# Kernel tuning notes

Measured on AMD Instinct MI355X. Metric: run time of the kernel, lower is better.

The kernel has to match this reference:

```python
import jax, jax.numpy as jnp
import numpy as np

EPS = 0.001  # numerical_stabilizer


def setup_inputs() -> dict:
    key = jax.random.key(0)
    ks = jax.random.split(key, 8)
    B, L, D, H, M = 4, 4096, 1024, 16, 64
    scale = 0.02
    return {
        "query": jax.random.normal(ks[0], (B, L, D), jnp.float32),
        "key": jax.random.normal(ks[1], (B, L, D), jnp.float32),
        "value": jax.random.normal(ks[2], (B, L, D), jnp.float32),
        "Wq": jax.random.normal(ks[3], (D, H, M), jnp.float32) * scale,
        "bq": jnp.zeros((H, M), jnp.float32),
        "Wk": jax.random.normal(ks[4], (D, H, M), jnp.float32) * scale,
        "bk": jnp.zeros((H, M), jnp.float32),
        "Wv": jax.random.normal(ks[5], (D, H, M), jnp.float32) * scale,
        "bv": jnp.zeros((H, M), jnp.float32),
        "Wo": jax.random.normal(ks[6], (H, M, D), jnp.float32) * scale,
        "bo": jnp.zeros((D,), jnp.float32),
        "step": 0,
    }


def reference(query, key, value, Wq, bq, Wk, bk, Wv, bv, Wo, bo, step):
    # QKV projections: [B,L,D] x [D,H,M] -> [B,L,H,M]
    q = jnp.einsum('bld,dhm->blhm', query, Wq) + bq
    k = jnp.einsum('bld,dhm->blhm', key, Wk) + bk
    v = jnp.einsum('bld,dhm->blhm', value, Wv) + bv
    # ReLU feature map with stabilizer
    q = jax.nn.relu(q) + EPS
    k = jax.nn.relu(k) + EPS
    # Linear (kernelized) attention: KV outer-product state [B,H,M,M]
    kvs = jnp.einsum('blhm,blhd->bhmd', k, v)
    a_v = jnp.einsum('blhm,bhmd->blhd', q, kvs)
    # Normalizer: sum of keys over sequence
    ks_sum = jnp.sum(k, axis=1)                       # [B,H,M]
    norm = jnp.einsum('blhm,bhm->blh', q, ks_sum)     # [B,L,H]
    a_v = a_v / norm[..., None]
    # Output projection over (head, head_dim) -> hidden
    out = jnp.einsum('blhm,hmd->bld', a_v, Wo) + bo
    return out
```

## Files before the change

### kernel.cpp

```cpp
#include <hip/hip_runtime.h>
#include <stdint.h>


typedef __bf16 bf16;
typedef __bf16 bf16x4 __attribute__((ext_vector_type(4)));
typedef __bf16 bf16x8 __attribute__((ext_vector_type(8)));
typedef float f32x4 __attribute__((ext_vector_type(4)));

#define MFMA_(a, b, c) __builtin_amdgcn_mfma_f32_16x16x32_bf16((a), (b), (c), 0, 0, 0)

static constexpr int BB   = 4;
static constexpr int LSEQ = 4096;
static constexpr int DIM  = 1024;
static constexpr int HH   = 16;
static constexpr float EPSF = 0.001f;

__device__ __forceinline__ void gload16(bf16* lds, const bf16* g) {
  __builtin_amdgcn_global_load_lds(
      (const __attribute__((address_space(1))) void*)g,
      (__attribute__((address_space(3))) void*)lds, 16, 0, 0);
}

__global__ void k_cvt(const float* __restrict__ q, const float* __restrict__ k,
                      const float* __restrict__ v, bf16* __restrict__ xb) {
  const int nchunk = 3 << 21;
  const int nthr = gridDim.x * blockDim.x;
  int c = blockIdx.x * blockDim.x + threadIdx.x;
  for (; c + nthr < nchunk; c += 2 * nthr) {
    const int c2 = c + nthr;
    const int t1 = c >> 21, t2 = c2 >> 21;
    const size_t o1 = (size_t)(c  & 0x1FFFFF) * 8;
    const size_t o2 = (size_t)(c2 & 0x1FFFFF) * 8;
    const float* s1 = (t1 == 0) ? q : (t1 == 1) ? k : v;
    const float* s2 = (t2 == 0) ? q : (t2 == 1) ? k : v;
    const f32x4 a0 = __builtin_nontemporal_load(reinterpret_cast<const f32x4*>(s1 + o1));
    const f32x4 a1 = __builtin_nontemporal_load(reinterpret_cast<const f32x4*>(s1 + o1) + 1);
    const f32x4 b0 = __builtin_nontemporal_load(reinterpret_cast<const f32x4*>(s2 + o2));
    const f32x4 b1 = __builtin_nontemporal_load(reinterpret_cast<const f32x4*>(s2 + o2) + 1);
    bf16x8 oa, ob;
#pragma unroll
    for (int j = 0; j < 4; ++j) { oa[j] = (bf16)a0[j]; oa[4 + j] = (bf16)a1[j]; }
#pragma unroll
    for (int j = 0; j < 4; ++j) { ob[j] = (bf16)b0[j]; ob[4 + j] = (bf16)b1[j]; }
    *reinterpret_cast<bf16x8*>(xb + (size_t)t1 * 16777216u + o1) = oa;
    *reinterpret_cast<bf16x8*>(xb + (size_t)t2 * 16777216u + o2) = ob;
  }
  if (c < nchunk) {
    const int t = c >> 21;
    const size_t off = (size_t)(c & 0x1FFFFF) * 8;
    const float* src = (t == 0) ? q : (t == 1) ? k : v;
    const f32x4 a = __builtin_nontemporal_load(reinterpret_cast<const f32x4*>(src + off));
    const f32x4 b = __builtin_nontemporal_load(reinterpret_cast<const f32x4*>(src + off) + 1);
    bf16x8 o;
#pragma unroll
    for (int j = 0; j < 4; ++j) { o[j] = (bf16)a[j]; o[4 + j] = (bf16)b[j]; }
    *reinterpret_cast<bf16x8*>(xb + (size_t)t * 16777216u + off) = o;
  }
}

__global__ void k_prep_w4(const float* __restrict__ W0, const float* __restrict__ W1,
                          const float* __restrict__ W2, const float* __restrict__ W3,
                          bf16* __restrict__ T0, bf16* __restrict__ T1,
                          bf16* __restrict__ T2, bf16* __restrict__ T3) {
  const float* W; bf16* T;
  switch (blockIdx.z) {
    case 0:  W = W0; T = T0; break;
    case 1:  W = W1; T = T1; break;
    case 2:  W = W2; T = T2; break;
    default: W = W3; T = T3; break;
  }
  __shared__ float t[32][33];
  const int tx = threadIdx.x & 31, ty = threadIdx.x >> 5;
  const int r0 = blockIdx.x * 32, c0 = blockIdx.y * 32;
#pragma unroll
  for (int j = 0; j < 32; j += 8)
    t[ty + j][tx] = W[(size_t)(r0 + ty + j) * DIM + c0 + tx];
  __syncthreads();
#pragma unroll
  for (int j = 0; j < 32; j += 8)
    T[(size_t)(c0 + ty + j) * DIM + r0 + tx] = (bf16)t[tx][ty + j];
}

__global__ void k_init_vt(bf16* __restrict__ vt) {
  const int c = blockIdx.x * 256 + threadIdx.x;
  const int l8 = c & 511;
  const int r  = (c >> 9) & 15;
  const int bh = c >> 13;
  const bf16 val = (r == 0) ? (bf16)1.0f : (bf16)0.0f;
  bf16x8 o;
#pragma unroll
  for (int j = 0; j < 8; ++j) o[j] = val;
  *reinterpret_cast<bf16x8*>(vt + ((size_t)bh * 80 + 64 + r) * LSEQ + l8 * 8) = o;
}

__device__ __forceinline__ void stage_half(bf16* As0, bf16* Bs0,
                                           const bf16* Ab, const bf16* Bb,
                                           int h, int w, int srow, int scol) {
  const int t = h >> 2, reg = h & 3, buf = t & 1;
  bf16* lds = ((reg < 2) ? As0 : Bs0) + buf * 16384 + (reg & 1) * 8192;
  const bf16* g = (reg < 2) ? Ab : Bb;
  const int rbase = (reg & 1) * 128;
#pragma unroll
  for (int rr = 0; rr < 2; ++rr) {
    const int row = rbase + (rr * 8 + w) * 8 + srow;
    gload16(lds + (rr * 8 + w) * 512, g + (size_t)row * DIM + t * 64 + scol);
  }
}

#define LDA(d, g, f)                                                                              \
  a[d][0] = *reinterpret_cast<const bf16x8*>(&As0[(g) * 16384 + (wm * 128 + (f) * 16 + lr) * 64 + col0]); \
  a[d][1] = *reinterpret_cast<const bf16x8*>(&As0[(g) * 16384 + (wm * 128 + (f) * 16 + lr) * 64 + col1]);
#define LDB(d, g, c)                                                                              \
  b[d][0] = *reinterpret_cast<const bf16x8*>(&Bs0[(g) * 16384 + (wn * 64 + (c) * 16 + lr) * 64 + col0]); \
  b[d][1] = *reinterpret_cast<const bf16x8*>(&Bs0[(g) * 16384 + (wn * 64 + (c) * 16 + lr) * 64 + col1]);
#define MM(fi, ci, fo, co)                                                                        \
  acc[fo][co] = MFMA_(a[fi][0], b[ci][0], acc[fo][co]);                                           \
  acc[fo][co] = MFMA_(a[fi][1], b[ci][1], acc[fo][co]);

#define PHASE(g, q, pidx)                                                                         \
  {                                                                                               \
    if ((q) == 0) { LDA(0, g, 0) LDA(1, g, 1) LDA(2, g, 2) LDA(3, g, 3)                           \
                    LDB(0, g, 0) LDB(1, g, 1) }                                                   \
    else if ((q) == 1) { LDB(0, g, 2) LDB(1, g, 3) }                                              \
    else if ((q) == 2) { LDA(0, g, 4) LDA(1, g, 5) LDA(2, g, 6) LDA(3, g, 7) }                    \
    else { LDB(0, g, 0) LDB(1, g, 1) }                                                            \
    const int hh = 8 * i + 5 + (pidx);                                                            \
    if (hh < 64) stage_half(As0, Bs0, Ab, Bb, hh, w, srow, scol);                                 \
    if ((pidx) == 3 || (pidx) == 7) {                                                             \
      if (i < 7) { asm volatile("s_waitcnt vmcnt(2)" ::: "memory"); }                             \
      else       { asm volatile("s_waitcnt vmcnt(0)" ::: "memory"); }                             \
    }                                                                                             \
    __builtin_amdgcn_sched_barrier(0);                                                            \
    __builtin_amdgcn_s_barrier();                                                                 \
    __builtin_amdgcn_sched_barrier(0);                                                            \
    __builtin_amdgcn_s_setprio(1);                                                                \
    if ((q) == 0) { MM(0, 0, 0, 0) MM(1, 0, 1, 0) MM(2, 0, 2, 0) MM(3, 0, 3, 0)                   \
                    MM(0, 1, 0, 1) MM(1, 1, 1, 1) MM(2, 1, 2, 1) MM(3, 1, 3, 1) }                 \
    else if ((q) == 1) { MM(0, 0, 0, 2) MM(1, 0, 1, 2) MM(2, 0, 2, 2) MM(3, 0, 3, 2)              \
                         MM(0, 1, 0, 3) MM(1, 1, 1, 3) MM(2, 1, 2, 3) MM(3, 1, 3, 3) }            \
    else if ((q) == 2) { MM(0, 0, 4, 2) MM(1, 0, 5, 2) MM(2, 0, 6, 2) MM(3, 0, 7, 2)              \
                         MM(0, 1, 4, 3) MM(1, 1, 5, 3) MM(2, 1, 6, 3) MM(3, 1, 7, 3) }            \
    else { MM(0, 0, 4, 0) MM(1, 0, 5, 0) MM(2, 0, 6, 0) MM(3, 0, 7, 0)                            \
           MM(0, 1, 4, 1) MM(1, 1, 5, 1) MM(2, 1, 6, 1) MM(3, 1, 7, 1) }                          \
    __builtin_amdgcn_s_setprio(0);                                                                \
    __builtin_amdgcn_sched_barrier(0);                                                            \
    __builtin_amdgcn_s_barrier();                                                                 \
    __builtin_amdgcn_sched_barrier(0);                                                            \
  }

template <int MODE>
__global__ __launch_bounds__(512, 2) void k_gemm256(const bf16* __restrict__ X,
                                                    const bf16* __restrict__ WT,
                                                    const float* __restrict__ bias,
                                                    void* __restrict__ outp) {
  __shared__ __align__(16) bf16 SH[65536];
  bf16* As0 = SH;
  bf16* Bs0 = SH + 32768;
  const int tid = threadIdx.x;
  const int lane = tid & 63, w = tid >> 6;
  const int wm = w >> 2, wn = w & 3;
  const int lr = lane & 15, lk = (lane >> 4) & 3;
  const int n0 = blockIdx.x * 256, c0 = blockIdx.y * 256;
  const int swz = (lr & 7) * 8;
  const int col0 = (lk * 8) ^ swz;
  const int col1 = (lk * 8 + 32) ^ swz;
  const int srow = lane >> 3;
  const int scol = (((lane & 7) ^ ((lane >> 3) & 7)) * 8);
  const bf16* Ab = X + (size_t)n0 * DIM;
  const bf16* Bb = WT + (size_t)c0 * DIM;

  f32x4 acc[8][4] = {};
  bf16x8 a[4][2], b[2][2];

#pragma unroll
  for (int h = 0; h < 5; ++h) stage_half(As0, Bs0, Ab, Bb, h, w, srow, scol);
  asm volatile("s_waitcnt vmcnt(2)" ::: "memory");
  __builtin_amdgcn_sched_barrier(0);
  __builtin_amdgcn_s_barrier();
  __builtin_amdgcn_sched_barrier(0);

  for (int i = 0; i < 8; ++i) {
    PHASE(0, 0, 0) PHASE(0, 1, 1) PHASE(0, 2, 2) PHASE(0, 3, 3)
    PHASE(1, 0, 4) PHASE(1, 1, 5) PHASE(1, 2, 6) PHASE(1, 3, 7)
  }

  float bvv[4];
#pragma unroll
  for (int cb = 0; cb < 4; ++cb) bvv[cb] = bias[c0 + wn * 64 + cb * 16 + lr];
  const int bidx = n0 >> 12;
  const int l0 = n0 & (LSEQ - 1);

  if (MODE == 3) {
    float* out = (float*)outp;
#pragma unroll
    for (int f = 0; f < 8; ++f)
#pragma unroll
      for (int cb = 0; cb < 4; ++cb) {
        const int c = c0 + wn * 64 + cb * 16 + lr;
#pragma unroll
        for (int r = 0; r < 4; ++r) {
          const int row = n0 + wm * 128 + f * 16 + lk * 4 + r;
          out[(size_t)row * DIM + c] = acc[f][cb][r] + bvv[cb];
        }
      }
  } else if (MODE == 0) {
    __syncthreads();
#pragma unroll
    for (int f = 0; f < 8; ++f)
#pragma unroll
      for (int cb = 0; cb < 4; ++cb) {
        const int cl = wn * 64 + cb * 16 + lr;
#pragma unroll
        for (int r = 0; r < 4; ++r) {
          float x = acc[f][cb][r] + bvv[cb];
          x = fmaxf(x, 0.f) + EPSF;
          const int ll = wm * 128 + f * 16 + lk * 4 + r;
          SH[ll * 256 + ((((cl >> 3) ^ (ll & 7)) << 3) | (cl & 7))] = (bf16)x;
        }
      }
    __syncthreads();
    bf16* outb = (bf16*)outp;
#pragma unroll
    for (int it = 0; it < 16; ++it) {
      const int chunk = it * 512 + tid;
      const int row = chunk >> 5, blk = chunk & 31;
      const bf16x8 v = *reinterpret_cast<const bf16x8*>(&SH[row * 256 + ((blk ^ (row & 7)) << 3)]);
      *reinterpret_cast<bf16x8*>(outb + (size_t)(n0 + row) * DIM + c0 + blk * 8) = v;
    }
  } else {
    __syncthreads();
#pragma unroll
    for (int f = 0; f < 8; ++f)
#pragma unroll
      for (int cb = 0; cb < 4; ++cb) {
        const int cl = wn * 64 + cb * 16 + lr;
        const int ll = wm * 128 + f * 16 + lk * 4;
        bf16x4 o;
#pragma unroll
        for (int r = 0; r < 4; ++r) {
          float x = acc[f][cb][r] + bvv[cb];
          if (MODE == 1) x = fmaxf(x, 0.f) + EPSF;
          o[r] = (bf16)x;
        }
        *reinterpret_cast<bf16x4*>(
            &SH[cl * 256 + ((((ll >> 3) ^ (cl & 7)) << 3) | (ll & 7))]) = o;
      }
    __syncthreads();
    bf16* outb = (bf16*)outp;
#pragma unroll
    for (int it = 0; it < 16; ++it) {
      const int chunk = it * 512 + tid;
      const int row = chunk >> 5, blk = chunk & 31;
      const bf16x8 v = *reinterpret_cast<const bf16x8*>(&SH[row * 256 + ((blk ^ (row & 7)) << 3)]);
      const int cg = c0 + row;
      size_t rowbase;
      if (MODE == 1) rowbase = (size_t)bidx * 1024 + cg;
      else           rowbase = ((size_t)(bidx * HH + (cg >> 6)) * 80 + (cg & 63));
      *reinterpret_cast<bf16x8*>(outb + rowbase * LSEQ + l0 + blk * 8) = v;
    }
  }
}
#undef PHASE
#undef MM
#undef LDB
#undef LDA

__global__ __launch_bounds__(256, 2) void k_kvs(const bf16* __restrict__ kt,
                                                const bf16* __restrict__ vt,
                                                float* __restrict__ kvs) {
  const int tid = threadIdx.x, lane = tid & 63, wid = tid >> 6;
  const int lr = lane & 15, lk = lane >> 4;
  const int bh = blockIdx.y;
  const int lbase = blockIdx.x * 256;
  __shared__ bf16 As[64][64];
  __shared__ bf16 Bs[80][64];
  f32x4 acc[5] = {};
  const bf16* ktb = kt + (size_t)bh * 64 * LSEQ;
  const bf16* vtb = vt + (size_t)bh * 80 * LSEQ;

  for (int ks = 0; ks < 4; ++ks) {
    const int l0 = lbase + ks * 64;
    __syncthreads();
#pragma unroll
    for (int i = 0; i < 2; ++i) {
      const int e = i * 2048 + tid * 8;
      const int row = e >> 6, col = e & 63;
      *reinterpret_cast<bf16x8*>(&As[row][col]) =
          *reinterpret_cast<const bf16x8*>(ktb + (size_t)row * LSEQ + l0 + col);
    }
#pragma unroll
    for (int i = 0; i < 2; ++i) {
      const int e = i * 2048 + tid * 8;
      const int row = e >> 6, col = e & 63;
      *reinterpret_cast<bf16x8*>(&Bs[row][col]) =
          *reinterpret_cast<const bf16x8*>(vtb + (size_t)row * LSEQ + l0 + col);
    }
    if (tid < 128) {
      const int e = 4096 + tid * 8;
      const int row = e >> 6, col = e & 63;
      *reinterpret_cast<bf16x8*>(&Bs[row][col]) =
          *reinterpret_cast<const bf16x8*>(vtb + (size_t)row * LSEQ + l0 + col);
    }
    __syncthreads();
#pragma unroll
    for (int kk = 0; kk < 2; ++kk) {
      const bf16x8 af = *reinterpret_cast<const bf16x8*>(&As[wid * 16 + lr][kk * 32 + lk * 8]);
#pragma unroll
      for (int cb = 0; cb < 5; ++cb) {
        const bf16x8 bfr = *reinterpret_cast<const bf16x8*>(&Bs[cb * 16 + lr][kk * 32 + lk * 8]);
        acc[cb] = MFMA_(af, bfr, acc[cb]);
      }
    }
  }
  float* kb = kvs + (size_t)bh * 64 * 80;
#pragma unroll
  for (int cb = 0; cb < 5; ++cb) {
    const int dcol = cb * 16 + lr;
#pragma unroll
    for (int r = 0; r < 4; ++r) {
      const int m = wid * 16 + lk * 4 + r;
      atomicAdd(kb + m * 80 + dcol, acc[cb][r]);
    }
  }
}

__global__ void k_kvs_t(const float* __restrict__ kvs, bf16* __restrict__ bav) {
  const int bh = blockIdx.x;
  const float* src = kvs + (size_t)bh * 5120;
  bf16* dst = bav + (size_t)bh * 5120;
  for (int i = threadIdx.x; i < 5120; i += 256) {
    const int dp = i >> 6, mm = i & 63;
    dst[i] = (bf16)src[mm * 80 + dp];
  }
}

__global__ __launch_bounds__(256, 2) void k_av(const bf16* __restrict__ q,
                                               const bf16* __restrict__ bav,
                                               bf16* __restrict__ avn) {
  const int tid = threadIdx.x, lane = tid & 63, wid = tid >> 6;
  const int lr = lane & 15, lk = lane >> 4;
  const int bh = blockIdx.y, b = bh >> 4, h = bh & 15;
  const int l0 = blockIdx.x * 128;
  __shared__ bf16 As[128][64];
  __shared__ bf16 Bs[80][64];
  __shared__ float nrm[128];

  const bf16* qb = q + ((size_t)b * LSEQ + l0) * DIM + h * 64;
#pragma unroll
  for (int i = 0; i < 4; ++i) {
    const int e = i * 2048 + tid * 8;
    const int row = e >> 6, col = e & 63;
    *reinterpret_cast<bf16x8*>(&As[row][col]) =
        *reinterpret_cast<const bf16x8*>(qb + (size_t)row * DIM + col);
  }
  const bf16* bb = bav + (size_t)bh * 5120;
#pragma unroll
  for (int i = 0; i < 2; ++i) {
    const int e = i * 2048 + tid * 8;
    const int row = e >> 6, col = e & 63;
    *reinterpret_cast<bf16x8*>(&Bs[row][col]) =
        *reinterpret_cast<const bf16x8*>(bb + row * 64 + col);
  }
  if (tid < 128) {
    const int e = 4096 + tid * 8;
    const int row = e >> 6, col = e & 63;
    *reinterpret_cast<bf16x8*>(&Bs[row][col]) =
        *reinterpret_cast<const bf16x8*>(bb + row * 64 + col);
  }
  __syncthreads();

  f32x4 acc[2][5] = {};
#pragma unroll
  for (int kk = 0; kk < 2; ++kk) {
    bf16x8 af[2];
    af[0] = *reinterpret_cast<const bf16x8*>(&As[wid * 32 + lr][kk * 32 + lk * 8]);
    af[1] = *reinterpret_cast<const bf16x8*>(&As[wid * 32 + 16 + lr][kk * 32 + lk * 8]);
#pragma unroll
    for (int cb = 0; cb < 5; ++cb) {
      const bf16x8 bfr = *reinterpret_cast<const bf16x8*>(&Bs[cb * 16 + lr][kk * 32 + lk * 8]);
      acc[0][cb] = MFMA_(af[0], bfr, acc[0][cb]);
      acc[1][cb] = MFMA_(af[1], bfr, acc[1][cb]);
    }
  }
  if (lr == 0) {
#pragma unroll
    for (int rb = 0; rb < 2; ++rb)
#pragma unroll
      for (int r = 0; r < 4; ++r)
        nrm[wid * 32 + rb * 16 + lk * 4 + r] = acc[rb][4][r];
  }
  __syncthreads();
  bf16* ob = avn + ((size_t)b * LSEQ + l0) * DIM + h * 64;
#pragma unroll
  for (int rb = 0; rb < 2; ++rb) {
#pragma unroll
    for (int cb = 0; cb < 4; ++cb) {
#pragma unroll
      for (int r = 0; r < 4; ++r) {
        const int row = wid * 32 + rb * 16 + lk * 4 + r;
        const float x = acc[rb][cb][r] / nrm[row];
        ob[(size_t)row * DIM + cb * 16 + lr] = (bf16)x;
      }
    }
  }
}

extern "C" void kernel_launch(void* const* d_in, const int* in_sizes, int n_in,
                              void* d_out, int out_size, void* d_ws, size_t ws_size,
                              hipStream_t stream) {
  const float* query = (const float*)d_in[0];
  const float* key   = (const float*)d_in[1];
  const float* value = (const float*)d_in[2];
  const float* Wq    = (const float*)d_in[3];
  const float* bq    = (const float*)d_in[4];
  const float* Wk    = (const float*)d_in[5];
  const float* bk    = (const float*)d_in[6];
  const float* Wv    = (const float*)d_in[7];
  const float* bvp   = (const float*)d_in[8];
  const float* Wo    = (const float*)d_in[9];
  const float* bo    = (const float*)d_in[10];
  float* out = (float*)d_out;
  char* ws = (char*)d_ws;

  const size_t off_wqt = 0;
  const size_t off_wkt = off_wqt + (2u << 20);
  const size_t off_wvt = off_wkt + (2u << 20);
  const size_t off_wot = off_wvt + (2u << 20);
  const size_t off_xb  = off_wot + (2u << 20);
  const size_t off_vt  = off_xb  + 100663296ull;
  const size_t off_kvs = off_vt  + 41943040ull;
  const size_t off_bav = off_kvs + 1310720ull;
  const size_t total   = off_bav + 655360ull;
  if (ws_size < total) return;

  bf16*  WQT = (bf16*)(ws + off_wqt);
  bf16*  WKT = (bf16*)(ws + off_wkt);
  bf16*  WVT = (bf16*)(ws + off_wvt);
  bf16*  WOT = (bf16*)(ws + off_wot);
  bf16*  XB  = (bf16*)(ws + off_xb);
  bf16*  XBq = XB;
  bf16*  XBk = XB + 16777216u;
  bf16*  XBv = XB + 33554432u;
  bf16*  VT  = (bf16*)(ws + off_vt);
  float* KVS = (float*)(ws + off_kvs);
  bf16*  BAV = (bf16*)(ws + off_bav);
  bf16*  KT  = XBv;
  bf16*  Qb  = XBk;
  bf16*  AV  = XBq;

  k_cvt<<<2048, 256, 0, stream>>>(query, key, value, XB);
  k_prep_w4<<<dim3(32, 32, 4), 256, 0, stream>>>(Wq, Wk, Wv, Wo, WQT, WKT, WVT, WOT);
  k_init_vt<<<2048, 256, 0, stream>>>(VT);
  (void)hipMemsetAsync(KVS, 0, 1310720ull, stream);

  k_gemm256<2><<<dim3(64, 4), 512, 0, stream>>>(XBv, WVT, bvp, VT);
  k_gemm256<1><<<dim3(64, 4), 512, 0, stream>>>(XBk, WKT, bk, KT);
  k_gemm256<0><<<dim3(64, 4), 512, 0, stream>>>(XBq, WQT, bq, Qb);

  k_kvs<<<dim3(16, 64), 256, 0, stream>>>(KT, VT, KVS);
  k_kvs_t<<<64, 256, 0, stream>>>(KVS, BAV);

  k_av<<<dim3(32, 64), 256, 0, stream>>>(Qb, BAV, AV);

  k_gemm256<3><<<dim3(64, 4), 512, 0, stream>>>(AV, WOT, bo, out);
}
```

Measured before the change: 256.8 us.

## Deepen GEMM prefetch, hold full A/B fragments in registers, simplify convert loop

The 256x256 GEMM mainloop now loads all 8 A fragments and 4 B fragments into registers in the first two phases, so the later phases issue MFMAs with no LDS reads. The prefetch distance grows from 5 to 7 half-tiles, with the vmcnt waits changed to match, and stage_half now stages B before A. The aim is to cut LDS read traffic and hide more global-load latency. This raises register pressure under launch_bounds(512,2), which could cause spills or lower occupancy. The input conversion kernel also drops its manual two-chunk unrolling in favour of a plain grid-stride loop.

```diff
diff --git a/kernel.cpp b/kernel.cpp
--- a/kernel.cpp
+++ b/kernel.cpp
@@ -24,36 +24,17 @@
 __global__ void k_cvt(const float* __restrict__ q, const float* __restrict__ k,
                       const float* __restrict__ v, bf16* __restrict__ xb) {
   const int nchunk = 3 << 21;
-  const int nthr = gridDim.x * blockDim.x;
-  int c = blockIdx.x * blockDim.x + threadIdx.x;
-  for (; c + nthr < nchunk; c += 2 * nthr) {
-    const int c2 = c + nthr;
-    const int t1 = c >> 21, t2 = c2 >> 21;
-    const size_t o1 = (size_t)(c  & 0x1FFFFF) * 8;
-    const size_t o2 = (size_t)(c2 & 0x1FFFFF) * 8;
-    const float* s1 = (t1 == 0) ? q : (t1 == 1) ? k : v;
-    const float* s2 = (t2 == 0) ? q : (t2 == 1) ? k : v;
-    const f32x4 a0 = __builtin_nontemporal_load(reinterpret_cast<const f32x4*>(s1 + o1));
-    const f32x4 a1 = __builtin_nontemporal_load(reinterpret_cast<const f32x4*>(s1 + o1) + 1);
-    const f32x4 b0 = __builtin_nontemporal_load(reinterpret_cast<const f32x4*>(s2 + o2));
-    const f32x4 b1 = __builtin_nontemporal_load(reinterpret_cast<const f32x4*>(s2 + o2) + 1);
-    bf16x8 oa, ob;
-#pragma unroll
-    for (int j = 0; j < 4; ++j) { oa[j] = (bf16)a0[j]; oa[4 + j] = (bf16)a1[j]; }
-#pragma unroll
-    for (int j = 0; j < 4; ++j) { ob[j] = (bf16)b0[j]; ob[4 + j] = (bf16)b1[j]; }
-    *reinterpret_cast<bf16x8*>(xb + (size_t)t1 * 16777216u + o1) = oa;
-    *reinterpret_cast<bf16x8*>(xb + (size_t)t2 * 16777216u + o2) = ob;
-  }
-  if (c < nchunk) {
+  const int stride = gridDim.x * blockDim.x;
+  for (int c = blockIdx.x * blockDim.x + threadIdx.x; c < nchunk; c += stride) {
     const int t = c >> 21;
-    const size_t off = (size_t)(c & 0x1FFFFF) * 8;
+    const size_t off = (size_t)(c & ((1 << 21) - 1)) * 8;
     const float* src = (t == 0) ? q : (t == 1) ? k : v;
-    const f32x4 a = __builtin_nontemporal_load(reinterpret_cast<const f32x4*>(src + off));
-    const f32x4 b = __builtin_nontemporal_load(reinterpret_cast<const f32x4*>(src + off) + 1);
+    const f32x4* sp = reinterpret_cast<const f32x4*>(src + off);
+    const f32x4 a = __builtin_nontemporal_load(sp);
+    const f32x4 b = __builtin_nontemporal_load(sp + 1);
     bf16x8 o;
-#pragma unroll
-    for (int j = 0; j < 4; ++j) { o[j] = (bf16)a[j]; o[4 + j] = (bf16)b[j]; }
+    o[0] = (bf16)a[0]; o[1] = (bf16)a[1]; o[2] = (bf16)a[2]; o[3] = (bf16)a[3];
+    o[4] = (bf16)b[0]; o[5] = (bf16)b[1]; o[6] = (bf16)b[2]; o[7] = (bf16)b[3];
     *reinterpret_cast<bf16x8*>(xb + (size_t)t * 16777216u + off) = o;
   }
 }
@@ -97,8 +78,8 @@
                                            const bf16* Ab, const bf16* Bb,
                                            int h, int w, int srow, int scol) {
   const int t = h >> 2, reg = h & 3, buf = t & 1;
-  bf16* lds = ((reg < 2) ? As0 : Bs0) + buf * 16384 + (reg & 1) * 8192;
-  const bf16* g = (reg < 2) ? Ab : Bb;
+  bf16* lds = ((reg >= 2) ? As0 : Bs0) + buf * 16384 + (reg & 1) * 8192;
+  const bf16* g = (reg >= 2) ? Ab : Bb;
   const int rbase = (reg & 1) * 128;
 #pragma unroll
   for (int rr = 0; rr < 2; ++rr) {
@@ -120,14 +101,12 @@
 #define PHASE(g, q, pidx)                                                                         \
   {                                                                                               \
     if ((q) == 0) { LDA(0, g, 0) LDA(1, g, 1) LDA(2, g, 2) LDA(3, g, 3)                           \
-                    LDB(0, g, 0) LDB(1, g, 1) }                                                   \
-    else if ((q) == 1) { LDB(0, g, 2) LDB(1, g, 3) }                                              \
-    else if ((q) == 2) { LDA(0, g, 4) LDA(1, g, 5) LDA(2, g, 6) LDA(3, g, 7) }                    \
-    else { LDB(0, g, 0) LDB(1, g, 1) }                                                            \
-    const int hh = 8 * i + 5 + (pidx);                                                            \
+                    LDB(0, g, 0) LDB(1, g, 1) LDB(2, g, 2) LDB(3, g, 3) }                         \
+    else if ((q) == 1) { LDA(4, g, 4) LDA(5, g, 5) LDA(6, g, 6) LDA(7, g, 7) }                    \
+    const int hh = 8 * i + 7 + (pidx);                                                            \
     if (hh < 64) stage_half(As0, Bs0, Ab, Bb, hh, w, srow, scol);                                 \
     if ((pidx) == 3 || (pidx) == 7) {                                                             \
-      if (i < 7) { asm volatile("s_waitcnt vmcnt(2)" ::: "memory"); }                             \
+      if (i < 7) { asm volatile("s_waitcnt vmcnt(6)" ::: "memory"); }                             \
       else       { asm volatile("s_waitcnt vmcnt(0)" ::: "memory"); }                             \
     }                                                                                             \
     __builtin_amdgcn_sched_barrier(0);                                                            \
@@ -136,12 +115,12 @@
     __builtin_amdgcn_s_setprio(1);                                                                \
     if ((q) == 0) { MM(0, 0, 0, 0) MM(1, 0, 1, 0) MM(2, 0, 2, 0) MM(3, 0, 3, 0)                   \
                     MM(0, 1, 0, 1) MM(1, 1, 1, 1) MM(2, 1, 2, 1) MM(3, 1, 3, 1) }                 \
-    else if ((q) == 1) { MM(0, 0, 0, 2) MM(1, 0, 1, 2) MM(2, 0, 2, 2) MM(3, 0, 3, 2)              \
-                         MM(0, 1, 0, 3) MM(1, 1, 1, 3) MM(2, 1, 2, 3) MM(3, 1, 3, 3) }            \
-    else if ((q) == 2) { MM(0, 0, 4, 2) MM(1, 0, 5, 2) MM(2, 0, 6, 2) MM(3, 0, 7, 2)              \
-                         MM(0, 1, 4, 3) MM(1, 1, 5, 3) MM(2, 1, 6, 3) MM(3, 1, 7, 3) }            \
-    else { MM(0, 0, 4, 0) MM(1, 0, 5, 0) MM(2, 0, 6, 0) MM(3, 0, 7, 0)                            \
-           MM(0, 1, 4, 1) MM(1, 1, 5, 1) MM(2, 1, 6, 1) MM(3, 1, 7, 1) }                          \
+    else if ((q) == 1) { MM(0, 2, 0, 2) MM(1, 2, 1, 2) MM(2, 2, 2, 2) MM(3, 2, 3, 2)              \
+                         MM(0, 3, 0, 3) MM(1, 3, 1, 3) MM(2, 3, 2, 3) MM(3, 3, 3, 3) }            \
+    else if ((q) == 2) { MM(4, 2, 4, 2) MM(5, 2, 5, 2) MM(6, 2, 6, 2) MM(7, 2, 7, 2)              \
+                         MM(4, 3, 4, 3) MM(5, 3, 5, 3) MM(6, 3, 6, 3) MM(7, 3, 7, 3) }            \
+    else { MM(4, 0, 4, 0) MM(5, 0, 5, 0) MM(6, 0, 6, 0) MM(7, 0, 7, 0)                            \
+           MM(4, 1, 4, 1) MM(5, 1, 5, 1) MM(6, 1, 6, 1) MM(7, 1, 7, 1) }                          \
     __builtin_amdgcn_s_setprio(0);                                                                \
     __builtin_amdgcn_sched_barrier(0);                                                            \
     __builtin_amdgcn_s_barrier();                                                                 \
@@ -170,11 +149,11 @@
   const bf16* Bb = WT + (size_t)c0 * DIM;
 
   f32x4 acc[8][4] = {};
-  bf16x8 a[4][2], b[2][2];
-
-#pragma unroll
-  for (int h = 0; h < 5; ++h) stage_half(As0, Bs0, Ab, Bb, h, w, srow, scol);
-  asm volatile("s_waitcnt vmcnt(2)" ::: "memory");
+  bf16x8 a[8][2], b[4][2];
+
+#pragma unroll
+  for (int h = 0; h < 7; ++h) stage_half(As0, Bs0, Ab, Bb, h, w, srow, scol);
+  asm volatile("s_waitcnt vmcnt(6)" ::: "memory");
   __builtin_amdgcn_sched_barrier(0);
   __builtin_amdgcn_s_barrier();
   __builtin_amdgcn_sched_barrier(0);
```

Result: slower. 286.4 us (+11.5%).

## Fuse fp32-to-bf16 input conversion into the QKV projection GEMMs

Applied to the files above, without the earlier changes.

Removes the standalone conversion kernel that turned query, key and value into bf16 in a workspace buffer. A new projection GEMM instead loads the fp32 activations straight into registers, converts them, and writes the bf16 tile into swizzled LDS, while the weights still use async global-to-LDS loads. The aim is to drop the extra full write and re-read of the converted activations. In exchange, the fp32 inputs are fetched once per column block, twice the bytes per fetch. The new kernel also uses a simpler single-buffer loop with register prefetch instead of the tuned ping-pong MFMA pipeline.

```diff
diff --git a/kernel.cpp b/kernel.cpp
--- a/kernel.cpp
+++ b/kernel.cpp
@@ -19,43 +19,6 @@
   __builtin_amdgcn_global_load_lds(
       (const __attribute__((address_space(1))) void*)g,
       (__attribute__((address_space(3))) void*)lds, 16, 0, 0);
-}
-
-__global__ void k_cvt(const float* __restrict__ q, const float* __restrict__ k,
-                      const float* __restrict__ v, bf16* __restrict__ xb) {
-  const int nchunk = 3 << 21;
-  const int nthr = gridDim.x * blockDim.x;
-  int c = blockIdx.x * blockDim.x + threadIdx.x;
-  for (; c + nthr < nchunk; c += 2 * nthr) {
-    const int c2 = c + nthr;
-    const int t1 = c >> 21, t2 = c2 >> 21;
-    const size_t o1 = (size_t)(c  & 0x1FFFFF) * 8;
-    const size_t o2 = (size_t)(c2 & 0x1FFFFF) * 8;
-    const float* s1 = (t1 == 0) ? q : (t1 == 1) ? k : v;
-    const float* s2 = (t2 == 0) ? q : (t2 == 1) ? k : v;
-    const f32x4 a0 = __builtin_nontemporal_load(reinterpret_cast<const f32x4*>(s1 + o1));
-    const f32x4 a1 = __builtin_nontemporal_load(reinterpret_cast<const f32x4*>(s1 + o1) + 1);
-    const f32x4 b0 = __builtin_nontemporal_load(reinterpret_cast<const f32x4*>(s2 + o2));
-    const f32x4 b1 = __builtin_nontemporal_load(reinterpret_cast<const f32x4*>(s2 + o2) + 1);
-    bf16x8 oa, ob;
-#pragma unroll
-    for (int j = 0; j < 4; ++j) { oa[j] = (bf16)a0[j]; oa[4 + j] = (bf16)a1[j]; }
-#pragma unroll
-    for (int j = 0; j < 4; ++j) { ob[j] = (bf16)b0[j]; ob[4 + j] = (bf16)b1[j]; }
-    *reinterpret_cast<bf16x8*>(xb + (size_t)t1 * 16777216u + o1) = oa;
-    *reinterpret_cast<bf16x8*>(xb + (size_t)t2 * 16777216u + o2) = ob;
-  }
-  if (c < nchunk) {
-    const int t = c >> 21;
-    const size_t off = (size_t)(c & 0x1FFFFF) * 8;
-    const float* src = (t == 0) ? q : (t == 1) ? k : v;
-    const f32x4 a = __builtin_nontemporal_load(reinterpret_cast<const f32x4*>(src + off));
-    const f32x4 b = __builtin_nontemporal_load(reinterpret_cast<const f32x4*>(src + off) + 1);
-    bf16x8 o;
-#pragma unroll
-    for (int j = 0; j < 4; ++j) { o[j] = (bf16)a[j]; o[4 + j] = (bf16)b[j]; }
-    *reinterpret_cast<bf16x8*>(xb + (size_t)t * 16777216u + off) = o;
-  }
 }
 
 __global__ void k_prep_w4(const float* __restrict__ W0, const float* __restrict__ W1,
@@ -91,6 +54,146 @@
 #pragma unroll
   for (int j = 0; j < 8; ++j) o[j] = val;
   *reinterpret_cast<bf16x8*>(vt + ((size_t)bh * 80 + 64 + r) * LSEQ + l8 * 8) = o;
+}
+
+template <int MODE>
+__global__ __launch_bounds__(512, 2) void k_projf(const float* __restrict__ X,
+                                                  const bf16* __restrict__ WT,
+                                                  const float* __restrict__ bias,
+                                                  bf16* __restrict__ outp) {
+  __shared__ __align__(16) bf16 SH[65536];
+  bf16* As = SH;
+  bf16* Bs = SH + 16384;
+  const int tid = threadIdx.x;
+  const int lane = tid & 63, w = tid >> 6;
+  const int wm = w >> 2, wn = w & 3;
+  const int lr = lane & 15, lk = (lane >> 4) & 3;
+  const int n0 = blockIdx.x * 256, c0 = blockIdx.y * 256;
+  const int swz = (lr & 7) * 8;
+  const int col0 = (lk * 8) ^ swz;
+  const int col1 = (lk * 8 + 32) ^ swz;
+  const int srow = lane >> 3;
+  const int scol = (((lane & 7) ^ ((lane >> 3) & 7)) * 8);
+  const float* Xb = X + (size_t)n0 * DIM;
+  const bf16* Bb = WT + (size_t)c0 * DIM;
+
+  f32x4 acc[8][4] = {};
+  f32x4 af[8];
+  const int arow[1] = {0};  (void)arow;
+
+#pragma unroll
+  for (int j = 0; j < 8; ++j) {
+    const int idx = tid + j * 512, row = idx >> 4, c4 = idx & 15;
+    af[j] = __builtin_nontemporal_load(
+        reinterpret_cast<const f32x4*>(Xb + (size_t)row * DIM + c4 * 4));
+  }
+
+  for (int ks = 0; ks < 16; ++ks) {
+    const int k0 = ks * 64;
+    __syncthreads();
+#pragma unroll
+    for (int rr = 0; rr < 4; ++rr) {
+      const int row = (rr * 8 + w) * 8 + srow;
+      gload16(Bs + (rr * 8 + w) * 512, Bb + (size_t)row * DIM + k0 + scol);
+    }
+#pragma unroll
+    for (int j = 0; j < 8; ++j) {
+      const int idx = tid + j * 512, row = idx >> 4, c4 = idx & 15;
+      bf16x4 o;
+      o[0] = (bf16)af[j][0]; o[1] = (bf16)af[j][1];
+      o[2] = (bf16)af[j][2]; o[3] = (bf16)af[j][3];
+      *reinterpret_cast<bf16x4*>(
+          &As[row * 64 + ((((c4 >> 1) ^ (row & 7)) << 3) | ((c4 & 1) << 2))]) = o;
+    }
+    __syncthreads();
+    if (ks < 15) {
+#pragma unroll
+      for (int j = 0; j < 8; ++j) {
+        const int idx = tid + j * 512, row = idx >> 4, c4 = idx & 15;
+        af[j] = __builtin_nontemporal_load(
+            reinterpret_cast<const f32x4*>(Xb + (size_t)row * DIM + k0 + 64 + c4 * 4));
+      }
+    }
+    bf16x8 a[8][2], b[4][2];
+#pragma unroll
+    for (int f = 0; f < 8; ++f) {
+      a[f][0] = *reinterpret_cast<const bf16x8*>(&As[(wm * 128 + f * 16 + lr) * 64 + col0]);
+      a[f][1] = *reinterpret_cast<const bf16x8*>(&As[(wm * 128 + f * 16 + lr) * 64 + col1]);
+    }
+#pragma unroll
+    for (int cb = 0; cb < 4; ++cb) {
+      b[cb][0] = *reinterpret_cast<const bf16x8*>(&Bs[(wn * 64 + cb * 16 + lr) * 64 + col0]);
+      b[cb][1] = *reinterpret_cast<const bf16x8*>(&Bs[(wn * 64 + cb * 16 + lr) * 64 + col1]);
+    }
+#pragma unroll
+    for (int kk = 0; kk < 2; ++kk)
+#pragma unroll
+      for (int f = 0; f < 8; ++f)
+#pragma unroll
+        for (int cb = 0; cb < 4; ++cb)
+          acc[f][cb] = MFMA_(a[f][kk], b[cb][kk], acc[f][cb]);
+  }
+
+  float bvv[4];
+#pragma unroll
+  for (int cb = 0; cb < 4; ++cb) bvv[cb] = bias[c0 + wn * 64 + cb * 16 + lr];
+  const int bidx = n0 >> 12;
+  const int l0 = n0 & (LSEQ - 1);
+
+  if (MODE == 0) {
+    __syncthreads();
+#pragma unroll
+    for (int f = 0; f < 8; ++f)
+#pragma unroll
+      for (int cb = 0; cb < 4; ++cb) {
+        const int cl = wn * 64 + cb * 16 + lr;
+#pragma unroll
+        for (int r = 0; r < 4; ++r) {
+          float x = acc[f][cb][r] + bvv[cb];
+          x = fmaxf(x, 0.f) + EPSF;
+          const int ll = wm * 128 + f * 16 + lk * 4 + r;
+          SH[ll * 256 + ((((cl >> 3) ^ (ll & 7)) << 3) | (cl & 7))] = (bf16)x;
+        }
+      }
+    __syncthreads();
+#pragma unroll
+    for (int it = 0; it < 16; ++it) {
+      const int chunk = it * 512 + tid;
+      const int row = chunk >> 5, blk = chunk & 31;
+      const bf16x8 v = *reinterpret_cast<const bf16x8*>(&SH[row * 256 + ((blk ^ (row & 7)) << 3)]);
+      *reinterpret_cast<bf16x8*>(outp + (size_t)(n0 + row) * DIM + c0 + blk * 8) = v;
+    }
+  } else {
+    __syncthreads();
+#pragma unroll
+    for (int f = 0; f < 8; ++f)
+#pragma unroll
+      for (int cb = 0; cb < 4; ++cb) {
+        const int cl = wn * 64 + cb * 16 + lr;
+        const int ll = wm * 128 + f * 16 + lk * 4;
+        bf16x4 o;
+#pragma unroll
+        for (int r = 0; r < 4; ++r) {
+          float x = acc[f][cb][r] + bvv[cb];
+          if (MODE == 1) x = fmaxf(x, 0.f) + EPSF;
+          o[r] = (bf16)x;
+        }
+        *reinterpret_cast<bf16x4*>(
+            &SH[cl * 256 + ((((ll >> 3) ^ (cl & 7)) << 3) | (ll & 7))]) = o;
+      }
+    __syncthreads();
+#pragma unroll
+    for (int it = 0; it < 16; ++it) {
+      const int chunk = it * 512 + tid;
+      const int row = chunk >> 5, blk = chunk & 31;
+      const bf16x8 v = *reinterpret_cast<const bf16x8*>(&SH[row * 256 + ((blk ^ (row & 7)) << 3)]);
+      const int cg = c0 + row;
+      size_t rowbase;
+      if (MODE == 1) rowbase = (size_t)bidx * 1024 + cg;
+      else           rowbase = ((size_t)(bidx * HH + (cg >> 6)) * 80 + (cg & 63));
+      *reinterpret_cast<bf16x8*>(outp + rowbase * LSEQ + l0 + blk * 8) = v;
+    }
+  }
 }
 
 __device__ __forceinline__ void stage_half(bf16* As0, bf16* Bs0,
@@ -148,11 +251,10 @@
     __builtin_amdgcn_sched_barrier(0);                                                            \
   }
 
-template <int MODE>
 __global__ __launch_bounds__(512, 2) void k_gemm256(const bf16* __restrict__ X,
                                                     const bf16* __restrict__ WT,
                                                     const float* __restrict__ bias,
-                                                    void* __restrict__ outp) {
+                                                    float* __restrict__ outp) {
   __shared__ __align__(16) bf16 SH[65536];
   bf16* As0 = SH;
   bf16* Bs0 = SH + 32768;
@@ -187,78 +289,17 @@
   float bvv[4];
 #pragma unroll
   for (int cb = 0; cb < 4; ++cb) bvv[cb] = bias[c0 + wn * 64 + cb * 16 + lr];
-  const int bidx = n0 >> 12;
-  const int l0 = n0 & (LSEQ - 1);
-
-  if (MODE == 3) {
-    float* out = (float*)outp;
-#pragma unroll
-    for (int f = 0; f < 8; ++f)
-#pragma unroll
-      for (int cb = 0; cb < 4; ++cb) {
-        const int c = c0 + wn * 64 + cb * 16 + lr;
-#pragma unroll
-        for (int r = 0; r < 4; ++r) {
-          const int row = n0 + wm * 128 + f * 16 + lk * 4 + r;
-          out[(size_t)row * DIM + c] = acc[f][cb][r] + bvv[cb];
-        }
+#pragma unroll
+  for (int f = 0; f < 8; ++f)
+#pragma unroll
+    for (int cb = 0; cb < 4; ++cb) {
+      const int c = c0 + wn * 64 + cb * 16 + lr;
+#pragma unroll
+      for (int r = 0; r < 4; ++r) {
+        const int row = n0 + wm * 128 + f * 16 + lk * 4 + r;
+        outp[(size_t)row * DIM + c] = acc[f][cb][r] + bvv[cb];
       }
-  } else if (MODE == 0) {
-    __syncthreads();
-#pragma unroll
-    for (int f = 0; f < 8; ++f)
-#pragma unroll
-      for (int cb = 0; cb < 4; ++cb) {
-        const int cl = wn * 64 + cb * 16 + lr;
-#pragma unroll
-        for (int r = 0; r < 4; ++r) {
-          float x = acc[f][cb][r] + bvv[cb];
-          x = fmaxf(x, 0.f) + EPSF;
-          const int ll = wm * 128 + f * 16 + lk * 4 + r;
-          SH[ll * 256 + ((((cl >> 3) ^ (ll & 7)) << 3) | (cl & 7))] = (bf16)x;
-        }
-      }
-    __syncthreads();
-    bf16* outb = (bf16*)outp;
-#pragma unroll
-    for (int it = 0; it < 16; ++it) {
-      const int chunk = it * 512 + tid;
-      const int row = chunk >> 5, blk = chunk & 31;
-      const bf16x8 v = *reinterpret_cast<const bf16x8*>(&SH[row * 256 + ((blk ^ (row & 7)) << 3)]);
-      *reinterpret_cast<bf16x8*>(outb + (size_t)(n0 + row) * DIM + c0 + blk * 8) = v;
-    }
-  } else {
-    __syncthreads();
-#pragma unroll
-    for (int f = 0; f < 8; ++f)
-#pragma unroll
-      for (int cb = 0; cb < 4; ++cb) {
-        const int cl = wn * 64 + cb * 16 + lr;
-        const int ll = wm * 128 + f * 16 + lk * 4;
-        bf16x4 o;
-#pragma unroll
-        for (int r = 0; r < 4; ++r) {
-          float x = acc[f][cb][r] + bvv[cb];
-          if (MODE == 1) x = fmaxf(x, 0.f) + EPSF;
-          o[r] = (bf16)x;
-        }
-        *reinterpret_cast<bf16x4*>(
-            &SH[cl * 256 + ((((ll >> 3) ^ (cl & 7)) << 3) | (ll & 7))]) = o;
-      }
-    __syncthreads();
-    bf16* outb = (bf16*)outp;
-#pragma unroll
-    for (int it = 0; it < 16; ++it) {
-      const int chunk = it * 512 + tid;
-      const int row = chunk >> 5, blk = chunk & 31;
-      const bf16x8 v = *reinterpret_cast<const bf16x8*>(&SH[row * 256 + ((blk ^ (row & 7)) << 3)]);
-      const int cg = c0 + row;
-      size_t rowbase;
-      if (MODE == 1) rowbase = (size_t)bidx * 1024 + cg;
-      else           rowbase = ((size_t)(bidx * HH + (cg >> 6)) * 80 + (cg & 63));
-      *reinterpret_cast<bf16x8*>(outb + rowbase * LSEQ + l0 + blk * 8) = v;
-    }
-  }
+    }
 }
 #undef PHASE
 #undef MM
@@ -426,8 +467,10 @@
   const size_t off_wkt = off_wqt + (2u << 20);
   const size_t off_wvt = off_wkt + (2u << 20);
   const size_t off_wot = off_wvt + (2u << 20);
-  const size_t off_xb  = off_wot + (2u << 20);
-  const size_t off_vt  = off_xb  + 100663296ull;
+  const size_t off_kt  = off_wot + (2u << 20);
+  const size_t off_qb  = off_kt  + 33554432ull;
+  const size_t off_av  = off_qb  + 33554432ull;
+  const size_t off_vt  = off_av  + 33554432ull;
   const size_t off_kvs = off_vt  + 41943040ull;
   const size_t off_bav = off_kvs + 1310720ull;
   const size_t total   = off_bav + 655360ull;
@@ -437,30 +480,25 @@
   bf16*  WKT = (bf16*)(ws + off_wkt);
   bf16*  WVT = (bf16*)(ws + off_wvt);
   bf16*  WOT = (bf16*)(ws + off_wot);
-  bf16*  XB  = (bf16*)(ws + off_xb);
-  bf16*  XBq = XB;
-  bf16*  XBk = XB + 16777216u;
-  bf16*  XBv = XB + 33554432u;
+  bf16*  KT  = (bf16*)(ws + off_kt);
+  bf16*  Qb  = (bf16*)(ws + off_qb);
+  bf16*  AV  = (bf16*)(ws + off_av);
   bf16*  VT  = (bf16*)(ws + off_vt);
   float* KVS = (float*)(ws + off_kvs);
   bf16*  BAV = (bf16*)(ws + off_bav);
-  bf16*  KT  = XBv;
-  bf16*  Qb  = XBk;
-  bf16*  AV  = XBq;
-
-  k_cvt<<<2048, 256, 0, stream>>>(query, key, value, XB);
+
   k_prep_w4<<<dim3(32, 32, 4), 256, 0, stream>>>(Wq, Wk, Wv, Wo, WQT, WKT, WVT, WOT);
   k_init_vt<<<2048, 256, 0, stream>>>(VT);
   (void)hipMemsetAsync(KVS, 0, 1310720ull, stream);
 
-  k_gemm256<2><<<dim3(64, 4), 512, 0, stream>>>(XBv, WVT, bvp, VT);
-  k_gemm256<1><<<dim3(64, 4), 512, 0, stream>>>(XBk, WKT, bk, KT);
-  k_gemm256<0><<<dim3(64, 4), 512, 0, stream>>>(XBq, WQT, bq, Qb);
+  k_projf<2><<<dim3(64, 4), 512, 0, stream>>>(value, WVT, bvp, VT);
+  k_projf<1><<<dim3(64, 4), 512, 0, stream>>>(key,   WKT, bk, KT);
+  k_projf<0><<<dim3(64, 4), 512, 0, stream>>>(query, WQT, bq, Qb);
 
   k_kvs<<<dim3(16, 64), 256, 0, stream>>>(KT, VT, KVS);
   k_kvs_t<<<64, 256, 0, stream>>>(KVS, BAV);
 
   k_av<<<dim3(32, 64), 256, 0, stream>>>(Qb, BAV, AV);
 
-  k_gemm256<3><<<dim3(64, 4), 512, 0, stream>>>(AV, WOT, bo, out);
-}
+  k_gemm256<<<dim3(64, 4), 512, 0, stream>>>(AV, WOT, bo, out);
+}
```

New measurement: 251.7 us. 2.0% less time.
